# Optimization experiments

Measured on AMD Instinct MI355X. Metric: run time of the kernel, lower is better.

## Reference

```python
import jax, jax.numpy as jnp
import numpy as np

B, PLEN, D = 32, 1024, 256


def setup_inputs() -> dict:
    key = jax.random.key(0)
    ks = jax.random.split(key, 8)
    u = lambda k, shape: jax.random.uniform(k, shape, jnp.float32, -0.05, 0.05)
    return {
        "P": jax.random.normal(ks[0], (B, PLEN, D), jnp.float32),
        "w_itr_att": u(ks[1], (3 * D,)),
        "w1": u(ks[2], (2 * D, D)),
        "w2": u(ks[3], (2 * D, D)),
        "w3": u(ks[4], (2 * D, D)),
        "b1": u(ks[5], (D,)),
        "b2": u(ks[6], (D,)),
        "b3": u(ks[7], (D,)),
    }


def reference(P, w_itr_att, w1, w2, w3, b1, b2, b3):
    d = P.shape[-1]
    # alpha(a,b) = w_itr_att . [a ; b ; a*b]; split w into the three d-chunks
    wa, wb, wc = w_itr_att[:d], w_itr_att[d:2 * d], w_itr_att[2 * d:]
    # pairwise score A[b,i,j] = wa.P_i + wb.P_j + wc.(P_i * P_j)
    sa = P @ wa                                   # (b, p)
    sb = P @ wb                                   # (b, p)
    A = sa[:, :, None] + sb[:, None, :] + jnp.einsum('bid,bjd->bij', P * wc, P)
    itr_attn = jnp.einsum('bij,bjd->bid', jax.nn.softmax(A, axis=2), P)
    cat = jnp.concatenate([P, itr_attn], axis=-1)  # (b, p, 2d)
    z = jnp.tanh(cat @ w1 + b1)
    r = jax.nn.sigmoid(cat @ w2 + b2)
    f = jax.nn.sigmoid(cat @ w3 + b3)
    return r * P + f * z
```

## Files before the change

kernel.cpp:

```cpp
#include <hip/hip_runtime.h>
#include <hip/hip_bf16.h>

typedef unsigned short u16;
typedef unsigned int   u32;

using bf16x8 = __attribute__((ext_vector_type(8))) short;
using f32x4  = __attribute__((ext_vector_type(4))) float;

#define NB 32
#define NP 1024
#define ND 256

__device__ __forceinline__ u16 f2bf(float x){
  u32 u = __float_as_uint(x);
  u += 0x7FFFu + ((u >> 16) & 1u);
  return (u16)(u >> 16);
}

__device__ __forceinline__ float bf2f(u16 x){
  return __uint_as_float((u32)x << 16);
}

__device__ __forceinline__ void glds16(const void* g, void* l){
  __builtin_amdgcn_global_load_lds((const __attribute__((address_space(1))) void*)g,
                                   (__attribute__((address_space(3))) void*)l, 16, 0, 0);
}

__global__ void prep_pt(const float* __restrict__ P, const float* __restrict__ wi,
                        u16* __restrict__ Pbf, u16* __restrict__ PbfT,
                        float* __restrict__ sbv){
  const int b = blockIdx.y, jt = blockIdx.x;
  __shared__ __align__(16) u16 T[64][264];
  const int tid = threadIdx.x;
  const int row = tid >> 2;
  const int dq  = tid & 3;
  const size_t grow = (size_t)b * NP + jt * 64 + row;
  const float* prow = P + grow * ND;
  const float* wbp  = wi + ND;
  float s = 0.f;
  #pragma unroll
  for (int it = 0; it < 4; ++it){
    const int d0 = it * 64 + dq * 16;
    float4 a0 = *(const float4*)(prow + d0);
    float4 a1 = *(const float4*)(prow + d0 + 4);
    float4 a2 = *(const float4*)(prow + d0 + 8);
    float4 a3 = *(const float4*)(prow + d0 + 12);
    float4 w0 = *(const float4*)(wbp + d0);
    float4 w1 = *(const float4*)(wbp + d0 + 4);
    float4 w2 = *(const float4*)(wbp + d0 + 8);
    float4 w3 = *(const float4*)(wbp + d0 + 12);
    s += a0.x*w0.x + a0.y*w0.y + a0.z*w0.z + a0.w*w0.w;
    s += a1.x*w1.x + a1.y*w1.y + a1.z*w1.z + a1.w*w1.w;
    s += a2.x*w2.x + a2.y*w2.y + a2.z*w2.z + a2.w*w2.w;
    s += a3.x*w3.x + a3.y*w3.y + a3.z*w3.z + a3.w*w3.w;
    u16 tmp[16];
    tmp[0]=f2bf(a0.x); tmp[1]=f2bf(a0.y); tmp[2]=f2bf(a0.z); tmp[3]=f2bf(a0.w);
    tmp[4]=f2bf(a1.x); tmp[5]=f2bf(a1.y); tmp[6]=f2bf(a1.z); tmp[7]=f2bf(a1.w);
    tmp[8]=f2bf(a2.x); tmp[9]=f2bf(a2.y); tmp[10]=f2bf(a2.z); tmp[11]=f2bf(a2.w);
    tmp[12]=f2bf(a3.x); tmp[13]=f2bf(a3.y); tmp[14]=f2bf(a3.z); tmp[15]=f2bf(a3.w);
    *(uint4*)&T[row][d0]     = *(uint4*)tmp;
    *(uint4*)&T[row][d0 + 8] = *(uint4*)(tmp + 8);
    *(uint4*)(Pbf + grow * ND + d0)     = *(uint4*)tmp;
    *(uint4*)(Pbf + grow * ND + d0 + 8) = *(uint4*)(tmp + 8);
  }
  s += __shfl_xor(s, 1, 64);
  s += __shfl_xor(s, 2, 64);
  if (dq == 0) sbv[grow] = s;
  __syncthreads();
  #pragma unroll
  for (int it = 0; it < 8; ++it){
    int cc = tid + 256 * it;
    int d = cc >> 3, c8 = cc & 7;
    u16 tmp[8];
    #pragma unroll
    for (int k = 0; k < 8; ++k) tmp[k] = T[c8 * 8 + k][d];
    *(uint4*)(PbfT + ((size_t)b * ND + d) * NP + jt * 64 + c8 * 8) = *(uint4*)tmp;
  }
}

__global__ void prep_w(const float* __restrict__ w1, const float* __restrict__ w2,
                       const float* __restrict__ w3, u16* __restrict__ Wp){
  const int t = blockIdx.x;
  const float* w = (t < 16) ? w1 : ((t < 32) ? w2 : w3);
  const int tid = threadIdx.x;
  #pragma unroll
  for (int j = 0; j < 4; ++j){
    int item = tid + 256 * j;
    int c = item >> 6, lane = item & 63;
    int ncol = ((t & 15) << 4) + (lane & 15);
    int k0 = 32 * c + 8 * (lane >> 4);
    u16 tmp[8];
    #pragma unroll
    for (int e = 0; e < 8; ++e) tmp[e] = f2bf(w[(size_t)(k0 + e) * 256 + ncol]);
    *(uint4*)(Wp + ((size_t)(t * 16 + c) * 64 + lane) * 8) = *(uint4*)tmp;
  }
}

__launch_bounds__(256, 2)
__global__ void attn_kernel(const float* __restrict__ P, const float* __restrict__ wi,
                            const u16* __restrict__ Pbf, const u16* __restrict__ PbfT,
                            const float* __restrict__ sbv, u16* __restrict__ attnb){
  const int p    = blockIdx.x;
  const int bid  = ((p & 7) << 6) | (p >> 3);
  const int b    = bid >> 4;
  const int q0   = (bid & 15) << 6;
  const int tid  = threadIdx.x;
  const int wave = tid >> 6, lane = tid & 63, lo = lane & 15, hi = lane >> 4;

  __shared__ __align__(16) u16 KtA[64 * 256];
  __shared__ __align__(16) u16 VtA[256 * 64];
  __shared__ __align__(16) u16 Sp[4][16][72];
  char* KtB = (char*)KtA;
  char* VtB = (char*)VtA;

  bf16x8 qf[8];
  {
    const int qrow = q0 + wave * 16 + lo;
    const float* prow = P  + ((size_t)b * NP + qrow) * ND;
    const float* wcp  = wi + 512;
    #pragma unroll
    for (int c = 0; c < 8; ++c){
      const int d0 = 32 * c + 8 * hi;
      float4 a  = *(const float4*)(prow + d0);
      float4 a2 = *(const float4*)(prow + d0 + 4);
      float4 wa  = *(const float4*)(wcp + d0);
      float4 wa2 = *(const float4*)(wcp + d0 + 4);
      bf16x8 q;
      q[0]=(short)f2bf(a.x*wa.x);  q[1]=(short)f2bf(a.y*wa.y);
      q[2]=(short)f2bf(a.z*wa.z);  q[3]=(short)f2bf(a.w*wa.w);
      q[4]=(short)f2bf(a2.x*wa2.x); q[5]=(short)f2bf(a2.y*wa2.y);
      q[6]=(short)f2bf(a2.z*wa2.z); q[7]=(short)f2bf(a2.w*wa2.w);
      qf[c] = q;
    }
  }

  f32x4 of[16];
  #pragma unroll
  for (int t = 0; t < 16; ++t) of[t] = (f32x4){0.f,0.f,0.f,0.f};
  float mx[4] = {-1e30f,-1e30f,-1e30f,-1e30f};
  float ls[4] = {0.f,0.f,0.f,0.f};

  const u16* kslab = Pbf  + (size_t)b * NP * ND;
  const u16* vslab = PbfT + (size_t)b * ND * NP;

  auto stageK = [&](int kt){
    const int kbase = kt * 64;
    #pragma unroll
    for (int it = 0; it < 8; ++it){
      int off = it * 4096 + tid * 16;
      int j   = off >> 9;
      int ck  = ((off >> 4) & 31) ^ (j & 7);
      glds16((const char*)(kslab + (size_t)(kbase + j) * ND + ck * 8), KtB + off);
    }
  };
  auto stageV = [&](int kt){
    const int kbase = kt * 64;
    #pragma unroll
    for (int it = 0; it < 8; ++it){
      int off = it * 4096 + tid * 16;
      int d   = off >> 7;
      int kc  = ((off >> 4) & 7) ^ (d & 7);
      glds16((const char*)(vslab + (size_t)d * NP + kbase + kc * 8), VtB + off);
    }
  };

  float sbc[4], sbn[4];
  stageK(0);
  stageV(0);
  #pragma unroll
  for (int nt = 0; nt < 4; ++nt) sbc[nt] = sbv[(size_t)b * NP + nt * 16 + lo];
  __syncthreads();

  for (int kt = 0; kt < 16; ++kt){
    f32x4 s[4];
    #pragma unroll
    for (int nt = 0; nt < 4; ++nt){
      f32x4 acc = (f32x4){0.f,0.f,0.f,0.f};
      #pragma unroll
      for (int c = 0; c < 8; ++c){
        int j  = nt * 16 + lo;
        int ad = j * 512 + (((4 * c + hi) ^ (j & 7)) << 4);
        bf16x8 kf = *(const bf16x8*)(KtB + ad);
        acc = __builtin_amdgcn_mfma_f32_16x16x32_bf16(qf[c], kf, acc, 0, 0, 0);
      }
      s[nt] = acc;
      float sv = sbc[nt];
      #pragma unroll
      for (int r = 0; r < 4; ++r) s[nt][r] += sv;
    }

    __syncthreads();
    if (kt < 15) stageK(kt + 1);

    float md = -1e30f;
    #pragma unroll
    for (int nt = 0; nt < 4; ++nt)
      #pragma unroll
      for (int r = 0; r < 4; ++r) md = fmaxf(md, s[nt][r] - mx[r]);
    if (!__all(md <= 8.f)){
      float scale[4];
      #pragma unroll
      for (int r = 0; r < 4; ++r){
        float v = fmaxf(fmaxf(s[0][r], s[1][r]), fmaxf(s[2][r], s[3][r]));
        v = fmaxf(v, __shfl_xor(v, 1, 64));
        v = fmaxf(v, __shfl_xor(v, 2, 64));
        v = fmaxf(v, __shfl_xor(v, 4, 64));
        v = fmaxf(v, __shfl_xor(v, 8, 64));
        float mnew = fmaxf(mx[r], v);
        scale[r] = __expf(mx[r] - mnew);
        mx[r] = mnew;
        ls[r] *= scale[r];
      }
      #pragma unroll
      for (int t = 0; t < 16; ++t)
        #pragma unroll
        for (int r = 0; r < 4; ++r) of[t][r] *= scale[r];
    }
    #pragma unroll
    for (int nt = 0; nt < 4; ++nt)
      #pragma unroll
      for (int r = 0; r < 4; ++r){
        float pv = __expf(s[nt][r] - mx[r]);
        ls[r] += pv;
        Sp[wave][4 * hi + r][16 * nt + lo] = f2bf(pv);
      }

    #pragma unroll
    for (int kk = 0; kk < 2; ++kk){
      bf16x8 pa = *(const bf16x8*)&Sp[wave][lo][32 * kk + 8 * hi];
      #pragma unroll
      for (int t = 0; t < 16; ++t){
        int d  = 16 * t + lo;
        int ad = d * 128 + (((4 * kk + hi) ^ (d & 7)) << 4);
        bf16x8 vb = *(const bf16x8*)(VtB + ad);
        of[t] = __builtin_amdgcn_mfma_f32_16x16x32_bf16(pa, vb, of[t], 0, 0, 0);
      }
    }

    __syncthreads();
    if (kt < 15){
      stageV(kt + 1);
      #pragma unroll
      for (int nt = 0; nt < 4; ++nt)
        sbn[nt] = sbv[(size_t)b * NP + (kt + 1) * 64 + nt * 16 + lo];
      sbc[0] = sbn[0]; sbc[1] = sbn[1]; sbc[2] = sbn[2]; sbc[3] = sbn[3];
    }
  }

  #pragma unroll
  for (int r = 0; r < 4; ++r){
    ls[r] += __shfl_xor(ls[r], 1, 64);
    ls[r] += __shfl_xor(ls[r], 2, 64);
    ls[r] += __shfl_xor(ls[r], 4, 64);
    ls[r] += __shfl_xor(ls[r], 8, 64);
  }
  const int qrow = q0 + wave * 16;
  #pragma unroll
  for (int t = 0; t < 16; ++t){
    #pragma unroll
    for (int r = 0; r < 4; ++r){
      float o = of[t][r] / ls[r];
      attnb[((size_t)b * NP + qrow + 4 * hi + r) * ND + 16 * t + lo] = f2bf(o);
    }
  }
}

__launch_bounds__(256, 2)
__global__ void mlp_kernel(const u16* __restrict__ Pbf, const u16* __restrict__ attnb,
                           const u16* __restrict__ Wp,
                           const float* __restrict__ b1, const float* __restrict__ b2,
                           const float* __restrict__ b3, float* __restrict__ out){
  const int p    = blockIdx.x;
  const int swz  = ((p & 7) << 7) | (p >> 3);
  const int mt   = swz >> 2, cg = swz & 3;
  const int tid  = threadIdx.x;
  const int wave = tid >> 6, lane = tid & 63, lo = lane & 15, hi = lane >> 4;
  const int tq   = 4 * cg + wave;
  const int m0   = mt * 128;

  __shared__ __align__(16) u16 Ab[2][128 * 64];

  f32x4 acc[3][8];
  #pragma unroll
  for (int e = 0; e < 3; ++e)
    #pragma unroll
    for (int m = 0; m < 8; ++m) acc[e][m] = (f32x4){0.f,0.f,0.f,0.f};

  auto stage = [&](int s, int buf){
    const u16* xs = (s < 4) ? (Pbf   + (size_t)m0 * ND + s * 64)
                            : (attnb + (size_t)m0 * ND + (s - 4) * 64);
    char* dst = (char*)Ab[buf];
    #pragma unroll
    for (int it = 0; it < 4; ++it){
      int off = it * 4096 + wave * 1024 + lane * 16;
      int row = off >> 7;
      int cl  = (off & 127) ^ ((row & 7) << 4);
      glds16((const char*)(xs + (size_t)row * ND) + cl, dst + it * 4096 + wave * 1024);
    }
  };

  stage(0, 0);
  __syncthreads();

  for (int s = 0; s < 8; ++s){
    if (s < 7) stage(s + 1, (s + 1) & 1);
    const char* ab = (const char*)Ab[s & 1];
    #pragma unroll
    for (int cc = 0; cc < 2; ++cc){
      const int c = 2 * s + cc;
      bf16x8 wf[3];
      #pragma unroll
      for (int e = 0; e < 3; ++e)
        wf[e] = *(const bf16x8*)(Wp + ((size_t)((tq + 16 * e) * 16 + c) * 64 + lane) * 8);
      #pragma unroll
      for (int m = 0; m < 8; ++m){
        int row = 16 * m + lo;
        bf16x8 af = *(const bf16x8*)(ab + row * 128 + ((64 * cc + 16 * hi) ^ ((row & 7) << 4)));
        #pragma unroll
        for (int e = 0; e < 3; ++e)
          acc[e][m] = __builtin_amdgcn_mfma_f32_16x16x32_bf16(af, wf[e], acc[e][m], 0, 0, 0);
      }
    }
    __syncthreads();
  }

  const int d = 16 * tq + lo;
  const float bb1 = b1[d], bb2 = b2[d], bb3 = b3[d];
  #pragma unroll
  for (int m = 0; m < 8; ++m){
    #pragma unroll
    for (int r = 0; r < 4; ++r){
      const int row = m0 + 16 * m + 4 * hi + r;
      float y1 = acc[0][m][r] + bb1;
      float y2 = acc[1][m][r] + bb2;
      float y3 = acc[2][m][r] + bb3;
      float pv = bf2f(Pbf[(size_t)row * ND + d]);
      float e2 = __expf(2.f * y1);
      float z  = (e2 - 1.f) / (e2 + 1.f);
      float rr = 1.f / (1.f + __expf(-y2));
      float ff = 1.f / (1.f + __expf(-y3));
      out[(size_t)row * ND + d] = rr * pv + ff * z;
    }
  }
}

extern "C" void kernel_launch(void* const* d_in, const int* in_sizes, int n_in,
                              void* d_out, int out_size, void* d_ws, size_t ws_size,
                              hipStream_t stream){
  const float* P  = (const float*)d_in[0];
  const float* wi = (const float*)d_in[1];
  const float* w1 = (const float*)d_in[2];
  const float* w2 = (const float*)d_in[3];
  const float* w3 = (const float*)d_in[4];
  const float* b1 = (const float*)d_in[5];
  const float* b2 = (const float*)d_in[6];
  const float* b3 = (const float*)d_in[7];
  float* out = (float*)d_out;

  char* ws = (char*)d_ws;
  u16*   Pbf   = (u16*)  (ws);
  u16*   PbfT  = (u16*)  (ws + (16u << 20));
  u16*   attnb = (u16*)  (ws + (32u << 20));
  u16*   Wp    = (u16*)  (ws + (48u << 20));
  float* sbv   = (float*)(ws + (49u << 20));

  prep_pt<<<dim3(16, 32), 256, 0, stream>>>(P, wi, Pbf, PbfT, sbv);
  prep_w<<<48, 256, 0, stream>>>(w1, w2, w3, Wp);
  attn_kernel<<<512, 256, 0, stream>>>(P, wi, Pbf, PbfT, sbv, attnb);
  mlp_kernel<<<1024, 256, 0, stream>>>(Pbf, attnb, Wp, b1, b2, b3, out);
}
```

Baseline: 112.7 us.

## Split PV output by head-dim across waves, sharing softmax probs via LDS

The P·V stage now partitions work so each wave owns a 64-column slice of the output dimension across all 64 query rows, rather than all 256 columns for its own 16 rows. Each V fragment loaded from LDS is reused across four MFMAs (one per query tile), which cuts V shared-memory reads per wave. The cost is extra sharing: each wave's probabilities, rescale factors and fast-path flags are published to LDS and read by all waves, and the first barrier moves after the softmax. The final normalization also goes through LDS and needs an additional barrier.

```diff
diff --git a/kernel.cpp b/kernel.cpp
--- a/kernel.cpp
+++ b/kernel.cpp
@@ -110,6 +110,9 @@
   __shared__ __align__(16) u16 KtA[64 * 256];
   __shared__ __align__(16) u16 VtA[256 * 64];
   __shared__ __align__(16) u16 Sp[4][16][72];
+  __shared__ float sls[4][16];
+  __shared__ float lfin[64];
+  __shared__ u32 fastf[4];
   char* KtB = (char*)KtA;
   char* VtB = (char*)VtA;
 
@@ -134,9 +137,11 @@
     }
   }
 
-  f32x4 of[16];
-  #pragma unroll
-  for (int t = 0; t < 16; ++t) of[t] = (f32x4){0.f,0.f,0.f,0.f};
+  f32x4 of[4][4];
+  #pragma unroll
+  for (int qt = 0; qt < 4; ++qt)
+    #pragma unroll
+    for (int dt = 0; dt < 4; ++dt) of[qt][dt] = (f32x4){0.f,0.f,0.f,0.f};
   float mx[4] = {-1e30f,-1e30f,-1e30f,-1e30f};
   float ls[4] = {0.f,0.f,0.f,0.f};
 
@@ -189,32 +194,29 @@
       for (int r = 0; r < 4; ++r) s[nt][r] += sv;
     }
 
-    __syncthreads();
-    if (kt < 15) stageK(kt + 1);
-
-    float md = -1e30f;
-    #pragma unroll
-    for (int nt = 0; nt < 4; ++nt)
-      #pragma unroll
-      for (int r = 0; r < 4; ++r) md = fmaxf(md, s[nt][r] - mx[r]);
-    if (!__all(md <= 8.f)){
-      float scale[4];
-      #pragma unroll
-      for (int r = 0; r < 4; ++r){
-        float v = fmaxf(fmaxf(s[0][r], s[1][r]), fmaxf(s[2][r], s[3][r]));
-        v = fmaxf(v, __shfl_xor(v, 1, 64));
-        v = fmaxf(v, __shfl_xor(v, 2, 64));
-        v = fmaxf(v, __shfl_xor(v, 4, 64));
-        v = fmaxf(v, __shfl_xor(v, 8, 64));
-        float mnew = fmaxf(mx[r], v);
-        scale[r] = __expf(mx[r] - mnew);
-        mx[r] = mnew;
-        ls[r] *= scale[r];
-      }
-      #pragma unroll
-      for (int t = 0; t < 16; ++t)
+    float scale[4] = {1.f, 1.f, 1.f, 1.f};
+    int fast = 1;
+    {
+      float md = -1e30f;
+      #pragma unroll
+      for (int nt = 0; nt < 4; ++nt)
         #pragma unroll
-        for (int r = 0; r < 4; ++r) of[t][r] *= scale[r];
+        for (int r = 0; r < 4; ++r) md = fmaxf(md, s[nt][r] - mx[r]);
+      if (!__all(md <= 8.f)){
+        fast = 0;
+        #pragma unroll
+        for (int r = 0; r < 4; ++r){
+          float v = fmaxf(fmaxf(s[0][r], s[1][r]), fmaxf(s[2][r], s[3][r]));
+          v = fmaxf(v, __shfl_xor(v, 1, 64));
+          v = fmaxf(v, __shfl_xor(v, 2, 64));
+          v = fmaxf(v, __shfl_xor(v, 4, 64));
+          v = fmaxf(v, __shfl_xor(v, 8, 64));
+          float mnew = fmaxf(mx[r], v);
+          scale[r] = __expf(mx[r] - mnew);
+          mx[r] = mnew;
+          ls[r] *= scale[r];
+        }
+      }
     }
     #pragma unroll
     for (int nt = 0; nt < 4; ++nt)
@@ -224,16 +226,41 @@
         ls[r] += pv;
         Sp[wave][4 * hi + r][16 * nt + lo] = f2bf(pv);
       }
+    if (lane == 0) fastf[wave] = (u32)fast;
+    if (lo == 0){
+      #pragma unroll
+      for (int r = 0; r < 4; ++r) sls[wave][4 * hi + r] = scale[r];
+    }
+
+    __syncthreads();
+    if (kt < 15) stageK(kt + 1);
+
+    if (!(fastf[0] & fastf[1] & fastf[2] & fastf[3])){
+      #pragma unroll
+      for (int qt = 0; qt < 4; ++qt){
+        #pragma unroll
+        for (int r = 0; r < 4; ++r){
+          float sc = sls[qt][4 * hi + r];
+          #pragma unroll
+          for (int dt = 0; dt < 4; ++dt) of[qt][dt][r] *= sc;
+        }
+      }
+    }
 
     #pragma unroll
     for (int kk = 0; kk < 2; ++kk){
-      bf16x8 pa = *(const bf16x8*)&Sp[wave][lo][32 * kk + 8 * hi];
-      #pragma unroll
-      for (int t = 0; t < 16; ++t){
-        int d  = 16 * t + lo;
+      bf16x8 pa[4];
+      #pragma unroll
+      for (int qt = 0; qt < 4; ++qt)
+        pa[qt] = *(const bf16x8*)&Sp[qt][lo][32 * kk + 8 * hi];
+      #pragma unroll
+      for (int dt = 0; dt < 4; ++dt){
+        int d  = wave * 64 + dt * 16 + lo;
         int ad = d * 128 + (((4 * kk + hi) ^ (d & 7)) << 4);
         bf16x8 vb = *(const bf16x8*)(VtB + ad);
-        of[t] = __builtin_amdgcn_mfma_f32_16x16x32_bf16(pa, vb, of[t], 0, 0, 0);
+        #pragma unroll
+        for (int qt = 0; qt < 4; ++qt)
+          of[qt][dt] = __builtin_amdgcn_mfma_f32_16x16x32_bf16(pa[qt], vb, of[qt][dt], 0, 0, 0);
       }
     }
 
@@ -254,13 +281,22 @@
     ls[r] += __shfl_xor(ls[r], 4, 64);
     ls[r] += __shfl_xor(ls[r], 8, 64);
   }
-  const int qrow = q0 + wave * 16;
-  #pragma unroll
-  for (int t = 0; t < 16; ++t){
+  if (lo == 0){
+    #pragma unroll
+    for (int r = 0; r < 4; ++r) lfin[wave * 16 + 4 * hi + r] = ls[r];
+  }
+  __syncthreads();
+  #pragma unroll
+  for (int qt = 0; qt < 4; ++qt){
     #pragma unroll
     for (int r = 0; r < 4; ++r){
-      float o = of[t][r] / ls[r];
-      attnb[((size_t)b * NP + qrow + 4 * hi + r) * ND + 16 * t + lo] = f2bf(o);
+      const float inv = 1.f / lfin[qt * 16 + 4 * hi + r];
+      const int qrow = q0 + qt * 16 + 4 * hi + r;
+      #pragma unroll
+      for (int dt = 0; dt < 4; ++dt){
+        float o = of[qt][dt][r] * inv;
+        attnb[((size_t)b * NP + qrow) * ND + wave * 64 + dt * 16 + lo] = f2bf(o);
+      }
     }
   }
 }
```

After: 109.0 us. -3.2%, faster.
